# Performance work log

Hardware: AMD Instinct MI355X
Metric: run time of the kernel (lower is better)

Reference implementation:

```python
import jax, jax.numpy as jnp
import numpy as np

D_MODEL = 1024
NHEAD = 16
HEAD_DIM = D_MODEL // NHEAD
BSZ, SEQ = 4, 2048


def setup_inputs() -> dict:
    key = jax.random.key(0)
    ks = jax.random.split(key, 9)
    s = 1.0 / np.sqrt(D_MODEL)
    x = jax.random.normal(ks[0], (BSZ, SEQ, D_MODEL), dtype=jnp.float32)
    # True above the diagonal = masked (torch masked_fill semantics)
    causal_mask = jnp.triu(jnp.ones((SEQ, SEQ), dtype=jnp.bool_), k=1)
    def lin(k):
        kw, kb = jax.random.split(k)
        W = jax.random.uniform(kw, (D_MODEL, D_MODEL), jnp.float32, -s, s)
        b = jax.random.uniform(kb, (D_MODEL,), jnp.float32, -s, s)
        return W, b
    Wq, bq = lin(ks[1]); Wk, bk = lin(ks[2]); Wv, bv = lin(ks[3]); Wo, bo = lin(ks[4])
    return {"x": x, "causal_mask": causal_mask,
            "Wq": Wq, "bq": bq, "Wk": Wk, "bk": bk,
            "Wv": Wv, "bv": bv, "Wo": Wo, "bo": bo}


def reference(x, causal_mask, Wq, bq, Wk, bk, Wv, bv, Wo, bo):
    bsz, seq, _ = x.shape
    def heads(W, b):
        # torch Linear: x @ W.T + b, then split heads -> [b, h, s, d]
        y = jnp.einsum('bse,de->bsd', x, W) + b
        return y.reshape(bsz, seq, NHEAD, HEAD_DIM).transpose(0, 2, 1, 3)
    q = heads(Wq, bq)
    k = heads(Wk, bk)
    v = heads(Wv, bv)
    scores = jnp.einsum('bhsd,bhtd->bhst', q, k) / jnp.sqrt(jnp.float32(HEAD_DIM))
    scores = jnp.where(causal_mask[None, None], -jnp.inf, scores)
    weights = jax.nn.softmax(scores, axis=-1)  # dropout p=0.0 -> identity
    ctx = jnp.einsum('bhst,bhtd->bhsd', weights, v)
    ctx = ctx.transpose(0, 2, 1, 3).reshape(bsz, seq, D_MODEL)
    return jnp.einsum('bsd,ed->bse', ctx, Wo) + bo
```

## Files before the change

kernel.cpp:

```cpp
#include <hip/hip_runtime.h>
#include <hip/hip_bf16.h>


typedef __bf16 bf16x8 __attribute__((ext_vector_type(8)));
typedef __bf16 bf16x4 __attribute__((ext_vector_type(4)));
typedef float  f32x4  __attribute__((ext_vector_type(4)));

#define SEQ 2048
#define NH  16
#define HD  64
#define DM  1024
#define RS  72

static __device__ __forceinline__ void gload_lds16(const __hip_bfloat16* g,
                                                   __hip_bfloat16* l) {
    __builtin_amdgcn_global_load_lds(
        (const __attribute__((address_space(1))) void*)g,
        (__attribute__((address_space(3))) void*)l, 16, 0, 0);
}

__global__ void detect_dtype_kernel(const unsigned short* __restrict__ x,
                                    int* __restrict__ flag) {
    if (threadIdx.x == 0 && blockIdx.x == 0) {
        int cnt = 0;
        for (int i = 0; i < 256; i += 2) {
            unsigned e = (x[i] >> 7) & 0xFFu;
            cnt += (e >= 0x70u && e <= 0x82u) ? 1 : 0;
        }
        *flag = (cnt >= 64) ? 0 : 1;
    }
}

__global__ __launch_bounds__(256) void cast4_kernel(
    const void* __restrict__ src, __hip_bfloat16* __restrict__ dst,
    const int* __restrict__ flag, int n4)
{
    const int i = blockIdx.x * 256 + threadIdx.x;
    if (i >= n4) return;
    bf16x4 o;
    if (*flag) {
        f32x4 f = ((const f32x4*)src)[i];
        #pragma unroll
        for (int j = 0; j < 4; ++j) o[j] = (__bf16)f[j];
    } else {
        o = ((const bf16x4*)src)[i];
    }
    ((bf16x4*)dst)[i] = o;
}

__global__ __launch_bounds__(256) void cast4x3_kernel(
    const void* s0, const void* s1, const void* s2,
    __hip_bfloat16* d0, __hip_bfloat16* d1, __hip_bfloat16* d2,
    const int* __restrict__ flag, int n4)
{
    const int i = blockIdx.x * 256 + threadIdx.x;
    if (i >= n4) return;
    const void* s = (blockIdx.y == 0) ? s0 : (blockIdx.y == 1) ? s1 : s2;
    __hip_bfloat16* d = (blockIdx.y == 0) ? d0 : (blockIdx.y == 1) ? d1 : d2;
    bf16x4 o;
    if (*flag) {
        f32x4 f = ((const f32x4*)s)[i];
        #pragma unroll
        for (int j = 0; j < 4; ++j) o[j] = (__bf16)f[j];
    } else {
        o = ((const bf16x4*)s)[i];
    }
    ((bf16x4*)d)[i] = o;
}

__global__ __launch_bounds__(256) void transpose_v_kernel(
    const __hip_bfloat16* __restrict__ v, __hip_bfloat16* __restrict__ vt)
{
    __shared__ __hip_bfloat16 T[HD * RS];
    const int tid = threadIdx.x;
    const int t0 = blockIdx.x * 64;
    const int h  = blockIdx.y;
    const int b  = blockIdx.z;

    const int tl = tid >> 3;
    const int d0 = (tid & 7) * 8;
    const __hip_bfloat16* vb = v + (size_t)b * SEQ * DM + (size_t)h * HD;
    bf16x8 a = *(const bf16x8*)(vb + (size_t)(t0 + tl) * DM + d0);
    bf16x8 c = *(const bf16x8*)(vb + (size_t)(t0 + tl + 32) * DM + d0);
    #pragma unroll
    for (int j = 0; j < 8; ++j) {
        T[(d0 + j) * RS + tl]      = __hip_bfloat16(a[j]);
        T[(d0 + j) * RS + tl + 32] = __hip_bfloat16(c[j]);
    }
    __syncthreads();
    const int dd = tid >> 3;
    const int tc = (tid & 7) * 8;
    __hip_bfloat16* vtb = vt + (size_t)(b * NH + h) * HD * SEQ;
    *(bf16x8*)(vtb + (size_t)dd * SEQ + t0 + tc) =
        *(const bf16x8*)&T[dd * RS + tc];
    *(bf16x8*)(vtb + (size_t)(dd + 32) * SEQ + t0 + tc) =
        *(const bf16x8*)&T[(dd + 32) * RS + tc];
}

struct GemmCoord {
    int l15, g, wm, wn, r0, c0;
    int aRead, bRead;
};
static __device__ __forceinline__ GemmCoord gemm_coords() {
    GemmCoord c;
    const int tid = threadIdx.x;
    const int lane = tid & 63, wv = tid >> 6;
    c.l15 = lane & 15; c.g = lane >> 4;
    c.wm = wv >> 1;    c.wn = wv & 1;
    c.r0 = tid >> 2;   c.c0 = tid & 3;
    c.aRead = (c.wm * 64 + c.l15) * 32 + c.g * 8;
    c.bRead = (c.wn * 64 + c.l15) * 32 + c.g * 8;
    return c;
}

#define GEMM_BODY(Aptr, Bptr, m0v, n0v)                                        \
    __shared__ __hip_bfloat16 As[128 * 32];                                    \
    __shared__ __hip_bfloat16 Bs[128 * 32];                                    \
    const GemmCoord cc = gemm_coords();                                        \
    const int wv = threadIdx.x >> 6;                                           \
    const __hip_bfloat16* Ag0 = (Aptr) + (size_t)((m0v) + cc.r0) * DM + cc.c0 * 8;      \
    const __hip_bfloat16* Ag1 = (Aptr) + (size_t)((m0v) + cc.r0 + 64) * DM + cc.c0 * 8; \
    const __hip_bfloat16* Bg0 = (Bptr) + (size_t)((n0v) + cc.r0) * DM + cc.c0 * 8;      \
    const __hip_bfloat16* Bg1 = (Bptr) + (size_t)((n0v) + cc.r0 + 64) * DM + cc.c0 * 8; \
    __hip_bfloat16* AsD0 = As + 512 * wv;                                      \
    __hip_bfloat16* AsD1 = As + 2048 + 512 * wv;                               \
    __hip_bfloat16* BsD0 = Bs + 512 * wv;                                      \
    __hip_bfloat16* BsD1 = Bs + 2048 + 512 * wv;                               \
    f32x4 acc[4][4];                                                           \
    _Pragma("unroll") for (int i = 0; i < 4; ++i)                              \
        _Pragma("unroll") for (int j = 0; j < 4; ++j)                          \
            acc[i][j] = (f32x4){0.f, 0.f, 0.f, 0.f};                           \
    for (int kb = 0; kb < DM; kb += 32) {                                      \
        __syncthreads();                                                       \
        gload_lds16(Ag0 + kb, AsD0);                                           \
        gload_lds16(Ag1 + kb, AsD1);                                           \
        gload_lds16(Bg0 + kb, BsD0);                                           \
        gload_lds16(Bg1 + kb, BsD1);                                           \
        __syncthreads();                                                       \
        bf16x8 af[4], bfr[4];                                                  \
        _Pragma("unroll") for (int i = 0; i < 4; ++i)                          \
            af[i] = *reinterpret_cast<const bf16x8*>(&As[cc.aRead + i * 512]); \
        _Pragma("unroll") for (int j = 0; j < 4; ++j)                          \
            bfr[j] = *reinterpret_cast<const bf16x8*>(&Bs[cc.bRead + j * 512]);\
        _Pragma("unroll") for (int i = 0; i < 4; ++i)                          \
            _Pragma("unroll") for (int j = 0; j < 4; ++j)                      \
                acc[i][j] = __builtin_amdgcn_mfma_f32_16x16x32_bf16(           \
                    af[i], bfr[j], acc[i][j], 0, 0, 0);                        \
    }

__global__ __launch_bounds__(256) void gemm_qkv(
    const __hip_bfloat16* __restrict__ A,
    const __hip_bfloat16* __restrict__ Wb,
    const void* bq, const void* bk, const void* bv,
    __hip_bfloat16* q, __hip_bfloat16* kk, __hip_bfloat16* vv,
    const int* __restrict__ dflag)
{
    const int widx = blockIdx.y >> 3;
    const int m0 = blockIdx.x * 128;
    const int n0 = (blockIdx.y & 7) * 128;
    const __hip_bfloat16* B = Wb + (size_t)widx * DM * DM;
    const void* bias = (widx == 0) ? bq : (widx == 1) ? bk : bv;
    __hip_bfloat16* out = (widx == 0) ? q : (widx == 1) ? kk : vv;
    const bool f32 = (*dflag != 0);

    GEMM_BODY(A, B, m0, n0)

    #pragma unroll
    for (int j = 0; j < 4; ++j) {
        const int col = n0 + cc.wn * 64 + j * 16 + cc.l15;
        const float bvv = f32 ? ((const float*)bias)[col]
                              : __bfloat162float(((const __hip_bfloat16*)bias)[col]);
        #pragma unroll
        for (int i = 0; i < 4; ++i) {
            #pragma unroll
            for (int r = 0; r < 4; ++r) {
                const int row = m0 + cc.wm * 64 + i * 16 + cc.g * 4 + r;
                out[(size_t)row * DM + col] = __float2bfloat16(acc[i][j][r] + bvv);
            }
        }
    }
}

__global__ __launch_bounds__(256) void gemm_out(
    const __hip_bfloat16* __restrict__ A,
    const __hip_bfloat16* __restrict__ B,
    const void* bias, void* __restrict__ outv,
    const int* __restrict__ dflag)
{
    const int m0 = blockIdx.x * 128;
    const int n0 = blockIdx.y * 128;
    const bool f32 = (*dflag != 0);

    GEMM_BODY(A, B, m0, n0)

    #pragma unroll
    for (int j = 0; j < 4; ++j) {
        const int col = n0 + cc.wn * 64 + j * 16 + cc.l15;
        const float bvv = f32 ? ((const float*)bias)[col]
                              : __bfloat162float(((const __hip_bfloat16*)bias)[col]);
        #pragma unroll
        for (int i = 0; i < 4; ++i) {
            #pragma unroll
            for (int r = 0; r < 4; ++r) {
                const int row = m0 + cc.wm * 64 + i * 16 + cc.g * 4 + r;
                const float val = acc[i][j][r] + bvv;
                if (f32) ((float*)outv)[(size_t)row * DM + col] = val;
                else ((__hip_bfloat16*)outv)[(size_t)row * DM + col] = __float2bfloat16(val);
            }
        }
    }
}

__global__ __launch_bounds__(256) void attn_flash_mfma(
    const __hip_bfloat16* __restrict__ q,
    const __hip_bfloat16* __restrict__ k,
    const __hip_bfloat16* __restrict__ vt,
    __hip_bfloat16* __restrict__ ctx)
{
    __shared__ __hip_bfloat16 Ks[64 * HD];
    __shared__ __hip_bfloat16 Vs[HD * 64];
    __shared__ __hip_bfloat16 P[4][16 * RS];

    const int tid  = threadIdx.x;
    const int lane = tid & 63;
    const int wave = tid >> 6;
    const int g    = lane >> 4;
    const int l15  = lane & 15;
    const int l7   = l15 & 7;

    const int lid  = blockIdx.x;
    const int xcd  = lid & 7;
    const int slot = lid >> 3;
    const int p    = (slot >> 4) * 8 + xcd;
    const int qp   = slot & 15;
    const int b    = p >> 4;
    const int h    = p & 15;

    const size_t hb = (size_t)b * SEQ * DM + (size_t)h * HD;
    const __hip_bfloat16* vth = vt + (size_t)(b * NH + h) * HD * SEQ;
    __hip_bfloat16* Pw = P[wave];

    const int c0  = wave * 64 + lane;
    const int c1  = 256 + wave * 64 + lane;
    const int kr0 = c0 >> 3, ks0 = ((c0 & 7) ^ (kr0 & 7)) * 8;
    const int kr1 = c1 >> 3, ks1 = ((c1 & 7) ^ (kr1 & 7)) * 8;
    __hip_bfloat16* KsD0 = Ks + wave * 512;
    __hip_bfloat16* KsD1 = Ks + 2048 + wave * 512;
    __hip_bfloat16* VsD0 = Vs + wave * 512;
    __hip_bfloat16* VsD1 = Vs + 2048 + wave * 512;

    const int f0off = ((g ^ l7)) * 8;
    const int f1off = (((4 + g) ^ l7)) * 8;

    bf16x8 ones;
    #pragma unroll
    for (int j = 0; j < 8; ++j) ones[j] = (__bf16)1.0f;

    #pragma unroll
    for (int half = 0; half < 2; ++half) {
        const int qt = half ? (SEQ / 64 - 1 - qp) : qp;
        const int q0 = qt * 64;

        const int qrow = q0 + wave * 16 + l15;
        const __hip_bfloat16* qp_ = q + hb + (size_t)qrow * DM + g * 8;
        bf16x8 qf0 = *reinterpret_cast<const bf16x8*>(qp_);
        bf16x8 qf1 = *reinterpret_cast<const bf16x8*>(qp_ + 32);
        #pragma unroll
        for (int j = 0; j < 8; ++j) {
            qf0[j] = (__bf16)((float)qf0[j] * 0.125f);
            qf1[j] = (__bf16)((float)qf1[j] * 0.125f);
        }

        f32x4 o[4];
        #pragma unroll
        for (int j = 0; j < 4; ++j) o[j] = (f32x4){0.f, 0.f, 0.f, 0.f};
        f32x4 zl = (f32x4){0.f, 0.f, 0.f, 0.f};

        for (int kt = 0; kt <= qt; ++kt) {
            const int kbase = kt * 64;

            __syncthreads();
            gload_lds16(k + hb + (size_t)(kbase + kr0) * DM + ks0, KsD0);
            gload_lds16(k + hb + (size_t)(kbase + kr1) * DM + ks1, KsD1);
            gload_lds16(vth + (size_t)kr0 * SEQ + kbase + ks0, VsD0);
            gload_lds16(vth + (size_t)kr1 * SEQ + kbase + ks1, VsD1);
            __syncthreads();

            f32x4 s[4];
            #pragma unroll
            for (int j = 0; j < 4; ++j) {
                const int krow = (j * 16 + l15) * 64;
                bf16x8 kf0 = *reinterpret_cast<const bf16x8*>(&Ks[krow + f0off]);
                bf16x8 kf1 = *reinterpret_cast<const bf16x8*>(&Ks[krow + f1off]);
                f32x4 z = (f32x4){0.f, 0.f, 0.f, 0.f};
                z = __builtin_amdgcn_mfma_f32_16x16x32_bf16(qf0, kf0, z, 0, 0, 0);
                z = __builtin_amdgcn_mfma_f32_16x16x32_bf16(qf1, kf1, z, 0, 0, 0);
                s[j] = z;
            }

            if (kt == qt) {
                #pragma unroll
                for (int j = 0; j < 4; ++j) {
                    const int key = j * 16 + l15;
                    #pragma unroll
                    for (int r = 0; r < 4; ++r) {
                        const int qq = wave * 16 + g * 4 + r;
                        if (key > qq) s[j][r] = -1e30f;
                    }
                }
            }

            #pragma unroll
            for (int j = 0; j < 4; ++j)
                #pragma unroll
                for (int r = 0; r < 4; ++r)
                    s[j][r] = __expf(s[j][r]);

            #pragma unroll
            for (int j = 0; j < 4; ++j)
                #pragma unroll
                for (int r = 0; r < 4; ++r)
                    Pw[(g * 4 + r) * RS + j * 16 + l15] = __float2bfloat16(s[j][r]);

            const bf16x8 a0 = *reinterpret_cast<const bf16x8*>(&Pw[l15 * RS + g * 8]);
            const bf16x8 a1 = *reinterpret_cast<const bf16x8*>(&Pw[l15 * RS + 32 + g * 8]);

            zl = __builtin_amdgcn_mfma_f32_16x16x32_bf16(a0, ones, zl, 0, 0, 0);
            zl = __builtin_amdgcn_mfma_f32_16x16x32_bf16(a1, ones, zl, 0, 0, 0);

            #pragma unroll
            for (int jd = 0; jd < 4; ++jd) {
                const int vrow = (jd * 16 + l15) * 64;
                const bf16x8 b0 = *reinterpret_cast<const bf16x8*>(&Vs[vrow + f0off]);
                const bf16x8 b1 = *reinterpret_cast<const bf16x8*>(&Vs[vrow + f1off]);
                o[jd] = __builtin_amdgcn_mfma_f32_16x16x32_bf16(a0, b0, o[jd], 0, 0, 0);
                o[jd] = __builtin_amdgcn_mfma_f32_16x16x32_bf16(a1, b1, o[jd], 0, 0, 0);
            }
        }

        #pragma unroll
        for (int r = 0; r < 4; ++r) {
            const float inv = 1.f / zl[r];
            const int sq = q0 + wave * 16 + g * 4 + r;
            #pragma unroll
            for (int jd = 0; jd < 4; ++jd)
                ctx[hb + (size_t)sq * DM + jd * 16 + l15] =
                    __float2bfloat16(o[jd][r] * inv);
        }
    }
}

extern "C" void kernel_launch(void* const* d_in, const int* in_sizes, int n_in,
                              void* d_out, int out_size, void* d_ws, size_t ws_size,
                              hipStream_t stream) {
    const int M = 4 * SEQ;

    int xi = 0, wi[4] = {-1, -1, -1, -1}, bi[4] = {-1, -1, -1, -1};
    int nw = 0, nb = 0;
    for (int i = 0; i < n_in; ++i) {
        if (in_sizes[i] == 4 * SEQ * DM) xi = i;
        else if (in_sizes[i] == DM * DM && nw < 4) wi[nw++] = i;
        else if (in_sizes[i] == DM && nb < 4) bi[nb++] = i;
    }
    if (nw < 4 || nb < 4) {
        const int wOff = n_in - 8;
        for (int j = 0; j < 4; ++j) { wi[j] = wOff + 2 * j; bi[j] = wOff + 2 * j + 1; }
    }
    const void* x  = d_in[xi];
    const void* W[4]  = {d_in[wi[0]], d_in[wi[1]], d_in[wi[2]], d_in[wi[3]]};
    const void* Bs[4] = {d_in[bi[0]], d_in[bi[1]], d_in[bi[2]], d_in[bi[3]]};

    const size_t mat = (size_t)M * DM;
    __hip_bfloat16* q   = (__hip_bfloat16*)d_ws;
    __hip_bfloat16* kk  = q + mat;
    __hip_bfloat16* vv  = kk + mat;
    __hip_bfloat16* ctx = q;
    int* flag = (int*)((char*)d_ws + 3 * mat * sizeof(__hip_bfloat16));

    __hip_bfloat16* xb  = (__hip_bfloat16*)d_out;
    __hip_bfloat16* wb  = xb + mat;
    __hip_bfloat16* vt  = (__hip_bfloat16*)d_out;
    __hip_bfloat16* wob = kk;

    detect_dtype_kernel<<<1, 64, 0, stream>>>((const unsigned short*)x, flag);

    cast4_kernel<<<dim3((int)(mat / 4 / 256)), 256, 0, stream>>>(x, xb, flag, (int)(mat / 4));
    cast4x3_kernel<<<dim3(DM * DM / 4 / 256, 3), 256, 0, stream>>>(
        W[0], W[1], W[2], wb, wb + (size_t)DM * DM, wb + 2 * (size_t)DM * DM,
        flag, DM * DM / 4);

    gemm_qkv<<<dim3(M / 128, 24), 256, 0, stream>>>(
        xb, wb, Bs[0], Bs[1], Bs[2], q, kk, vv, flag);

    transpose_v_kernel<<<dim3(SEQ / 64, NH, 4), 256, 0, stream>>>(vv, vt);

    attn_flash_mfma<<<dim3(1024), 256, 0, stream>>>(q, kk, vt, ctx);

    cast4_kernel<<<dim3(DM * DM / 4 / 256), 256, 0, stream>>>(W[3], wob, flag, DM * DM / 4);

    gemm_out<<<dim3(M / 128, DM / 128), 256, 0, stream>>>(ctx, wob, Bs[3], d_out, flag);
}
```

Measured before the change: 299.7 us.

## Fuse V transpose into QKV GEMM epilogue and vectorize P stores

```diff
diff --git a/kernel.cpp b/kernel.cpp
--- a/kernel.cpp
+++ b/kernel.cpp
@@ -66,35 +66,6 @@
         o = ((const bf16x4*)s)[i];
     }
     ((bf16x4*)d)[i] = o;
-}
-
-__global__ __launch_bounds__(256) void transpose_v_kernel(
-    const __hip_bfloat16* __restrict__ v, __hip_bfloat16* __restrict__ vt)
-{
-    __shared__ __hip_bfloat16 T[HD * RS];
-    const int tid = threadIdx.x;
-    const int t0 = blockIdx.x * 64;
-    const int h  = blockIdx.y;
-    const int b  = blockIdx.z;
-
-    const int tl = tid >> 3;
-    const int d0 = (tid & 7) * 8;
-    const __hip_bfloat16* vb = v + (size_t)b * SEQ * DM + (size_t)h * HD;
-    bf16x8 a = *(const bf16x8*)(vb + (size_t)(t0 + tl) * DM + d0);
-    bf16x8 c = *(const bf16x8*)(vb + (size_t)(t0 + tl + 32) * DM + d0);
-    #pragma unroll
-    for (int j = 0; j < 8; ++j) {
-        T[(d0 + j) * RS + tl]      = __hip_bfloat16(a[j]);
-        T[(d0 + j) * RS + tl + 32] = __hip_bfloat16(c[j]);
-    }
-    __syncthreads();
-    const int dd = tid >> 3;
-    const int tc = (tid & 7) * 8;
-    __hip_bfloat16* vtb = vt + (size_t)(b * NH + h) * HD * SEQ;
-    *(bf16x8*)(vtb + (size_t)dd * SEQ + t0 + tc) =
-        *(const bf16x8*)&T[dd * RS + tc];
-    *(bf16x8*)(vtb + (size_t)(dd + 32) * SEQ + t0 + tc) =
-        *(const bf16x8*)&T[(dd + 32) * RS + tc];
 }
 
 struct GemmCoord {
@@ -152,7 +123,7 @@
     const __hip_bfloat16* __restrict__ A,
     const __hip_bfloat16* __restrict__ Wb,
     const void* bq, const void* bk, const void* bv,
-    __hip_bfloat16* q, __hip_bfloat16* kk, __hip_bfloat16* vv,
+    __hip_bfloat16* q, __hip_bfloat16* kk, __hip_bfloat16* vt,
     const int* __restrict__ dflag)
 {
     const int widx = blockIdx.y >> 3;
@@ -160,22 +131,43 @@
     const int n0 = (blockIdx.y & 7) * 128;
     const __hip_bfloat16* B = Wb + (size_t)widx * DM * DM;
     const void* bias = (widx == 0) ? bq : (widx == 1) ? bk : bv;
-    __hip_bfloat16* out = (widx == 0) ? q : (widx == 1) ? kk : vv;
     const bool f32 = (*dflag != 0);
 
     GEMM_BODY(A, B, m0, n0)
 
-    #pragma unroll
-    for (int j = 0; j < 4; ++j) {
-        const int col = n0 + cc.wn * 64 + j * 16 + cc.l15;
-        const float bvv = f32 ? ((const float*)bias)[col]
-                              : __bfloat162float(((const __hip_bfloat16*)bias)[col]);
-        #pragma unroll
-        for (int i = 0; i < 4; ++i) {
-            #pragma unroll
-            for (int r = 0; r < 4; ++r) {
-                const int row = m0 + cc.wm * 64 + i * 16 + cc.g * 4 + r;
-                out[(size_t)row * DM + col] = __float2bfloat16(acc[i][j][r] + bvv);
+    if (widx == 2) {
+        #pragma unroll
+        for (int j = 0; j < 4; ++j) {
+            const int col = n0 + cc.wn * 64 + j * 16 + cc.l15;
+            const float bvv = f32 ? ((const float*)bias)[col]
+                                  : __bfloat162float(((const __hip_bfloat16*)bias)[col]);
+            #pragma unroll
+            for (int i = 0; i < 4; ++i) {
+                const int row0 = m0 + cc.wm * 64 + i * 16 + cc.g * 4;
+                const int bb = row0 >> 11;
+                const int t  = row0 & 2047;
+                bf16x4 pv;
+                #pragma unroll
+                for (int r = 0; r < 4; ++r)
+                    pv[r] = (__bf16)(acc[i][j][r] + bvv);
+                *reinterpret_cast<bf16x4*>(
+                    vt + (size_t)(bb * 1024 + col) * SEQ + t) = pv;
+            }
+        }
+    } else {
+        __hip_bfloat16* out = (widx == 0) ? q : kk;
+        #pragma unroll
+        for (int j = 0; j < 4; ++j) {
+            const int col = n0 + cc.wn * 64 + j * 16 + cc.l15;
+            const float bvv = f32 ? ((const float*)bias)[col]
+                                  : __bfloat162float(((const __hip_bfloat16*)bias)[col]);
+            #pragma unroll
+            for (int i = 0; i < 4; ++i) {
+                #pragma unroll
+                for (int r = 0; r < 4; ++r) {
+                    const int row = m0 + cc.wm * 64 + i * 16 + cc.g * 4 + r;
+                    out[(size_t)row * DM + col] = __float2bfloat16(acc[i][j][r] + bvv);
+                }
             }
         }
     }
@@ -293,18 +285,18 @@
                 bf16x8 kf0 = *reinterpret_cast<const bf16x8*>(&Ks[krow + f0off]);
                 bf16x8 kf1 = *reinterpret_cast<const bf16x8*>(&Ks[krow + f1off]);
                 f32x4 z = (f32x4){0.f, 0.f, 0.f, 0.f};
-                z = __builtin_amdgcn_mfma_f32_16x16x32_bf16(qf0, kf0, z, 0, 0, 0);
-                z = __builtin_amdgcn_mfma_f32_16x16x32_bf16(qf1, kf1, z, 0, 0, 0);
+                z = __builtin_amdgcn_mfma_f32_16x16x32_bf16(kf0, qf0, z, 0, 0, 0);
+                z = __builtin_amdgcn_mfma_f32_16x16x32_bf16(kf1, qf1, z, 0, 0, 0);
                 s[j] = z;
             }
 
             if (kt == qt) {
+                const int qq = wave * 16 + l15;
                 #pragma unroll
                 for (int j = 0; j < 4; ++j) {
-                    const int key = j * 16 + l15;
                     #pragma unroll
                     for (int r = 0; r < 4; ++r) {
-                        const int qq = wave * 16 + g * 4 + r;
+                        const int key = j * 16 + g * 4 + r;
                         if (key > qq) s[j][r] = -1e30f;
                     }
                 }
@@ -317,10 +309,12 @@
                     s[j][r] = __expf(s[j][r]);
 
             #pragma unroll
-            for (int j = 0; j < 4; ++j)
-                #pragma unroll
-                for (int r = 0; r < 4; ++r)
-                    Pw[(g * 4 + r) * RS + j * 16 + l15] = __float2bfloat16(s[j][r]);
+            for (int j = 0; j < 4; ++j) {
+                bf16x4 pv;
+                #pragma unroll
+                for (int r = 0; r < 4; ++r) pv[r] = (__bf16)s[j][r];
+                *reinterpret_cast<bf16x4*>(&Pw[l15 * RS + j * 16 + g * 4]) = pv;
+            }
 
             const bf16x8 a0 = *reinterpret_cast<const bf16x8*>(&Pw[l15 * RS + g * 8]);
             const bf16x8 a1 = *reinterpret_cast<const bf16x8*>(&Pw[l15 * RS + 32 + g * 8]);
@@ -373,13 +367,12 @@
     const size_t mat = (size_t)M * DM;
     __hip_bfloat16* q   = (__hip_bfloat16*)d_ws;
     __hip_bfloat16* kk  = q + mat;
-    __hip_bfloat16* vv  = kk + mat;
+    __hip_bfloat16* vt  = kk + mat;
     __hip_bfloat16* ctx = q;
     int* flag = (int*)((char*)d_ws + 3 * mat * sizeof(__hip_bfloat16));
 
     __hip_bfloat16* xb  = (__hip_bfloat16*)d_out;
     __hip_bfloat16* wb  = xb + mat;
-    __hip_bfloat16* vt  = (__hip_bfloat16*)d_out;
     __hip_bfloat16* wob = kk;
 
     detect_dtype_kernel<<<1, 64, 0, stream>>>((const unsigned short*)x, flag);
@@ -390,9 +383,7 @@
         flag, DM * DM / 4);
 
     gemm_qkv<<<dim3(M / 128, 24), 256, 0, stream>>>(
-        xb, wb, Bs[0], Bs[1], Bs[2], q, kk, vv, flag);
-
-    transpose_v_kernel<<<dim3(SEQ / 64, NH, 4), 256, 0, stream>>>(vv, vt);
+        xb, wb, Bs[0], Bs[1], Bs[2], q, kk, vt, flag);
 
     attn_flash_mfma<<<dim3(1024), 256, 0, stream>>>(q, kk, vt, ctx);
 
```

After: 275.7 us. 8.0% less time.
